# Kernel optimization log

Hardware: AMD Instinct MI355X
Metric: run time of the kernel (lower is better)

The kernel has to match this reference:

```python
import jax, jax.numpy as jnp
import numpy as np
import math

B, A, D = 32, 100, 10000
HID = 256
NH = 4
OUT = 10000
NFREQ = 16
E = round(OUT * 0.5 / (A / 2))  # max_entries = 100
N = int(math.sqrt(D))           # 100 (row/col decode of flat index)
SCALE = math.sqrt(HID)
STEPS = 3


def swish(x):
    return x * jax.nn.sigmoid(x)


def setup_inputs() -> dict:
    key = jax.random.key(0)
    ks = jax.random.split(key, 16)
    s = 0.02
    p = lambda k, shape: jax.random.normal(k, shape, jnp.float32) * s
    vals = jax.random.normal(ks[0], (B, A, D), jnp.float32)
    keep = jax.random.uniform(ks[1], (B, A, D)) < (E / D)  # ~E nonzeros per (b, agent)
    x = vals * keep
    return {
        "x": x,
        "fourier_B": jax.random.normal(ks[2], (NFREQ, 2), jnp.float32),
        "enc_W1": p(ks[3], (HID, 1 + 2 * NFREQ)), "enc_b1": jnp.zeros((HID,), jnp.float32),
        "enc_W2": p(ks[4], (HID, HID)), "enc_b2": jnp.zeros((HID,), jnp.float32),
        "pad_token": jnp.zeros((HID,), jnp.float32),
        "comp_W1": p(ks[5], (2 * HID, E * HID)), "comp_b1": jnp.zeros((2 * HID,), jnp.float32),
        "comp_W2": p(ks[6], (HID, 2 * HID)), "comp_b2": jnp.zeros((HID,), jnp.float32),
        "connectivity": jax.random.normal(ks[7], (A, A), jnp.float32),
        "qW": p(ks[8], (NH, HID, HID)), "kW": p(ks[9], (NH, HID, HID)), "vW": p(ks[10], (NH, HID, HID)),
        "fp_W1": p(ks[11], (NH, HID, HID)), "fp_b1": jnp.zeros((NH, HID), jnp.float32),
        "fp_W2": p(ks[12], (NH, HID, HID)), "fp_b2": jnp.zeros((NH, HID), jnp.float32),
        "ln_g": jnp.ones((NH, HID), jnp.float32), "ln_b": jnp.zeros((NH, HID), jnp.float32),
        "out_W": p(ks[13], (OUT, HID)), "out_b": jnp.zeros((OUT,), jnp.float32),
    }


def reference(x, fourier_B, enc_W1, enc_b1, enc_W2, enc_b2, pad_token,
              comp_W1, comp_b1, comp_W2, comp_b2, connectivity,
              qW, kW, vW, fp_W1, fp_b1, fp_W2, fp_b2, ln_g, ln_b, out_W, out_b):
    # --- ragged gather of nonzero entries, truncated/padded to E per (b, agent) ---
    mask = x != 0                                                   # [B,A,D]
    # stable argsort puts nonzero positions first, in ascending flat-index order
    # (same order as torch .nonzero per batch row)
    idx = jnp.argsort(jnp.logical_not(mask), axis=-1, stable=True)[..., :E]  # [B,A,E]
    valid = jnp.take_along_axis(mask, idx, axis=-1)                 # [B,A,E]
    vals = jnp.take_along_axis(x, idx, axis=-1)[..., None]          # [B,A,E,1]
    coords = jnp.stack([idx // N, idx % N], axis=-1).astype(x.dtype)  # [B,A,E,2]
    # Fourier positional encoding
    proj = (2.0 * math.pi) * jnp.einsum('baec,fc->baef', coords, fourier_B)
    pos = jnp.concatenate([jnp.sin(proj), jnp.cos(proj)], axis=-1)  # [B,A,E,2F]
    feat = jnp.concatenate([vals, pos], axis=-1)                    # [B,A,E,1+2F]
    # entry encoder MLP
    e = swish(feat @ enc_W1.T + enc_b1) @ enc_W2.T + enc_b2         # [B,A,E,HID]
    e = jnp.where(valid[..., None], e, pad_token)                   # pad slots -> pad_token
    # per-agent compression of the E entry embeddings
    flat = e.reshape(B, A, E * HID)
    h = swish(flat @ comp_W1.T + comp_b1) @ comp_W2.T + comp_b2     # [B,A,HID]

    # --- message passing: multi-head dot-product GAT with learned connectivity bias ---
    conn = connectivity[None, None]                                  # broadcast [1,1,A,A]
    for _ in range(STEPS):
        Q = jnp.einsum('bai,nji->nbaj', h, qW)                      # [NH,B,A,HID]
        K = jnp.einsum('bai,nji->nbaj', h, kW)
        V = jnp.einsum('bai,nji->nbaj', h, vW)
        scores = jnp.einsum('nbaj,nbcj->nbac', Q, K) / SCALE + conn
        alpha = jax.nn.softmax(scores, axis=-1)                     # dropout p=0.0
        Hm = jnp.einsum('nbac,nbcj->nbaj', alpha, V)
        t = jnp.einsum('nbaj,nij->nbai', swish(Hm), fp_W1) + fp_b1[:, None, None, :]
        t = jnp.einsum('nbaj,nij->nbai', swish(t), fp_W2) + fp_b2[:, None, None, :]
        m = t.mean(-1, keepdims=True)
        v = ((t - m) ** 2).mean(-1, keepdims=True)
        o = (t - m) / jnp.sqrt(v + 1e-5) * ln_g[:, None, None, :] + ln_b[:, None, None, :]
        h = o.mean(0)                                               # mean over heads

    return h @ out_W.T + out_b                                      # [B,A,OUT]
```

## Files before the change

### kernel.cpp

```cpp
#include <hip/hip_runtime.h>
#include <cstdint>
#include <cstddef>

#define NBATCH 32
#define NAGENT 100
#define NDIM   10000
#define HID    256
#define NHEAD  4
#define NOUT   10000
#define NFREQ  16
#define EMAX   100
#define NBA    3200
#define KBIG   25600
#define TWO_PI 6.283185307179586476925f

typedef float  v4f  __attribute__((ext_vector_type(4)));
typedef short  v8s  __attribute__((ext_vector_type(8)));

__device__ __forceinline__ unsigned short bf_hi(float f) {
    unsigned int u = __float_as_uint(f);
    return (unsigned short)((u + 0x7FFFu + ((u >> 16) & 1u)) >> 16);
}
__device__ __forceinline__ float bf_tof(unsigned short h) {
    return __uint_as_float(((unsigned int)h) << 16);
}

__global__ __launch_bounds__(64) void k_extract(const float* __restrict__ x,
                                                int* __restrict__ idxb,
                                                float* __restrict__ valb,
                                                int* __restrict__ nvalid)
{
    const int ba = blockIdx.x;
    const float* xr = x + (size_t)ba * NDIM;
    const int lane = threadIdx.x;
    int base = 0;
    for (int c0 = 0; c0 < NDIM; c0 += 64) {
        int i = c0 + lane;
        float v = (i < NDIM) ? xr[i] : 0.0f;
        unsigned long long m = __ballot(v != 0.0f);
        if (v != 0.0f) {
            int p = base + __popcll(m & ((1ull << lane) - 1ull));
            if (p < EMAX) {
                idxb[(size_t)ba * EMAX + p] = i;
                valb[(size_t)ba * EMAX + p] = v;
            }
        }
        base += __popcll(m);
        if (base >= EMAX) break;
    }
    if (lane == 0) nvalid[ba] = base < EMAX ? base : EMAX;
}

__global__ __launch_bounds__(256) void k_g1(
    const int* __restrict__ idxb, const float* __restrict__ valb,
    const int* __restrict__ nvalid, const float* __restrict__ fourB,
    const float* __restrict__ W1, const float* __restrict__ b1,
    unsigned short* __restrict__ g1h, unsigned short* __restrict__ g1l)
{
    __shared__ float s_feat[16][36];
    __shared__ float s_w[8448];
    __shared__ float s_b1v[256];
    __shared__ int   s_idx[16];
    __shared__ int   s_valid[16];

    const int t  = threadIdx.x;
    const int g0 = blockIdx.x * 16;

    if (t < 16) {
        int g = g0 + t;
        int ba = g / 100, slot = g - ba * 100;
        int valid = (slot < nvalid[ba]) ? 1 : 0;
        s_valid[t]   = valid;
        s_idx[t]     = valid ? idxb[g] : 0;
        s_feat[t][0] = valid ? valb[g] : 0.0f;
    }
    s_b1v[t] = b1[t];
    for (int i = t; i < 8448; i += 256) s_w[i] = W1[i];
    __syncthreads();

    {
        int ent = t >> 4, f = t & 15;
        float sv = 0.0f, cv = 0.0f;
        if (s_valid[ent]) {
            int id = s_idx[ent];
            float row = (float)(id / 100);
            float col = (float)(id % 100);
            float pr = TWO_PI * (row * fourB[2 * f] + col * fourB[2 * f + 1]);
            sv = sinf(pr); cv = cosf(pr);
        }
        s_feat[ent][1 + f]  = sv;
        s_feat[ent][17 + f] = cv;
    }
    __syncthreads();

    const float* wr = &s_w[t * 33];
    for (int ent = 0; ent < 16; ++ent) {
        float a = s_b1v[t];
        #pragma unroll
        for (int c = 0; c < 33; ++c) a += s_feat[ent][c] * wr[c];
        float g = a / (1.0f + expf(-a));
        g = s_valid[ent] ? g : 0.0f;
        unsigned short h = bf_hi(g);
        unsigned short l = bf_hi(g - bf_tof(h));
        size_t o = (size_t)(g0 + ent) * 256 + t;
        g1h[o] = h;
        g1l[o] = l;
    }
}

__global__ void k_w2t(const float* __restrict__ W2, float* __restrict__ W2T)
{
    int kp = blockIdx.x, k = threadIdx.x;
    W2T[kp * 256 + k] = W2[k * 256 + kp];
}

__global__ __launch_bounds__(256) void k_wsplit(const float* __restrict__ src,
                                                unsigned short* __restrict__ hi,
                                                unsigned short* __restrict__ lo)
{
    int i = (blockIdx.x * 256 + threadIdx.x) * 4;
    float4 f = *(const float4*)(src + i);
    ushort4 h, l;
    h.x = bf_hi(f.x); l.x = bf_hi(f.x - bf_tof(h.x));
    h.y = bf_hi(f.y); l.y = bf_hi(f.y - bf_tof(h.y));
    h.z = bf_hi(f.z); l.z = bf_hi(f.z - bf_tof(h.z));
    h.w = bf_hi(f.w); l.w = bf_hi(f.w - bf_tof(h.w));
    *(ushort4*)(hi + i) = h;
    *(ushort4*)(lo + i) = l;
}

__global__ __launch_bounds__(256) void k_tables(
    const float* __restrict__ W1, const float* __restrict__ pad,
    const float* __restrict__ b2, float* __restrict__ D, float* __restrict__ E0)
{
    __shared__ float red[4];
    const int n = blockIdx.x;
    const int t = threadIdx.x, lane = t & 63, w = t >> 6;
    const float pm = pad[t] - b2[t];
    const float bb = b2[t];
    const float* wr = W1 + (size_t)n * KBIG;
    float eb = 0.0f;
    for (int s = 0; s < 100; ++s) {
        float wv = wr[s * 256 + t];
        float p = pm * wv;
        eb += bb * wv;
        #pragma unroll
        for (int o = 32; o > 0; o >>= 1) p += __shfl_down(p, o);
        if (lane == 0) red[w] = p;
        __syncthreads();
        if (t == 0) D[s * 512 + n] = red[0] + red[1] + red[2] + red[3];
        __syncthreads();
    }
    #pragma unroll
    for (int o = 32; o > 0; o >>= 1) eb += __shfl_down(eb, o);
    if (lane == 0) red[w] = eb;
    __syncthreads();
    if (t == 0) E0[n] = red[0] + red[1] + red[2] + red[3];
}

__global__ void k_suffix(const float* __restrict__ D, float* __restrict__ Corr)
{
    int n = blockIdx.x * 256 + threadIdx.x;
    float c = 0.0f;
    Corr[100 * 512 + n] = 0.0f;
    for (int s = 99; s >= 0; --s) { c += D[s * 512 + n]; Corr[s * 512 + n] = c; }
}

template<int ACT>
__global__ __launch_bounds__(256) void k_gemmbf(
    const unsigned short* __restrict__ Ah, const unsigned short* __restrict__ Al,
    const unsigned short* __restrict__ Wh, const unsigned short* __restrict__ Wl,
    const float* __restrict__ bias, float* __restrict__ C,
    int M, int N, int K,
    long long sA, long long sW, long long sBias, long long sC)
{
    __shared__ unsigned short sA_h[4096], sA_l[4096], sW_h[4096], sW_l[4096];
    const int t = threadIdx.x;
    const int z = blockIdx.z;
    Ah += (size_t)z * sA;  Al += (size_t)z * sA;
    Wh += (size_t)z * sW;  Wl += (size_t)z * sW;
    C  += (size_t)z * sC;
    const float* bp = bias ? (bias + (size_t)z * sBias) : nullptr;
    const int bn = blockIdx.x * 128, bm = blockIdx.y * 128;
    const int lane = t & 63, w = t >> 6;
    const int wm = (w & 1) * 64, wn = (w >> 1) * 64;
    const int r0 = t >> 2, kq = (t & 3) * 8;
    const int r1 = 64 + r0;
    const uint4 zero4 = make_uint4(0u, 0u, 0u, 0u);

    const unsigned short* pA0 = Ah + (size_t)(bm + r0) * K + kq;
    const unsigned short* pA1 = Ah + (size_t)(bm + r1) * K + kq;
    const unsigned short* pa0 = Al + (size_t)(bm + r0) * K + kq;
    const unsigned short* pa1 = Al + (size_t)(bm + r1) * K + kq;
    const bool v0 = (bn + r0) < N, v1 = (bn + r1) < N;
    const unsigned short* pW0 = Wh + (size_t)(bn + r0) * K + kq;
    const unsigned short* pW1 = Wh + (size_t)(bn + r1) * K + kq;
    const unsigned short* pw0 = Wl + (size_t)(bn + r0) * K + kq;
    const unsigned short* pw1 = Wl + (size_t)(bn + r1) * K + kq;

    uint4 rA0 = *(const uint4*)pA0, rA1 = *(const uint4*)pA1;
    uint4 ra0 = *(const uint4*)pa0, ra1 = *(const uint4*)pa1;
    uint4 rW0 = v0 ? *(const uint4*)pW0 : zero4;
    uint4 rW1 = v1 ? *(const uint4*)pW1 : zero4;
    uint4 rw0 = v0 ? *(const uint4*)pw0 : zero4;
    uint4 rw1 = v1 ? *(const uint4*)pw1 : zero4;

    v4f acc[4][4] = {};
    const int i0 = (r0 * 32 + kq) ^ ((r0 & 7) << 3);
    const int i1 = (r1 * 32 + kq) ^ ((r1 & 7) << 3);
    const int KT = K >> 5;

    for (int kt = 0; kt < KT; ++kt) {
        __syncthreads();
        *(uint4*)&sA_h[i0] = rA0;  *(uint4*)&sA_h[i1] = rA1;
        *(uint4*)&sA_l[i0] = ra0;  *(uint4*)&sA_l[i1] = ra1;
        *(uint4*)&sW_h[i0] = rW0;  *(uint4*)&sW_h[i1] = rW1;
        *(uint4*)&sW_l[i0] = rw0;  *(uint4*)&sW_l[i1] = rw1;
        __syncthreads();
        if (kt + 1 < KT) {
            int o = (kt + 1) * 32;
            rA0 = *(const uint4*)(pA0 + o);  rA1 = *(const uint4*)(pA1 + o);
            ra0 = *(const uint4*)(pa0 + o);  ra1 = *(const uint4*)(pa1 + o);
            rW0 = v0 ? *(const uint4*)(pW0 + o) : zero4;
            rW1 = v1 ? *(const uint4*)(pW1 + o) : zero4;
            rw0 = v0 ? *(const uint4*)(pw0 + o) : zero4;
            rw1 = v1 ? *(const uint4*)(pw1 + o) : zero4;
        }
        const int fr = lane & 15, fq = (lane >> 4) * 8;
        v8s ahf[4], alf[4], bhf[4], blf[4];
        #pragma unroll
        for (int i = 0; i < 4; ++i) {
            int ar = wm + i * 16 + fr;
            int br = wn + i * 16 + fr;
            int ai = (ar * 32 + fq) ^ ((ar & 7) << 3);
            int bi = (br * 32 + fq) ^ ((br & 7) << 3);
            ahf[i] = *(const v8s*)&sA_h[ai];
            alf[i] = *(const v8s*)&sA_l[ai];
            bhf[i] = *(const v8s*)&sW_h[bi];
            blf[i] = *(const v8s*)&sW_l[bi];
        }
        #pragma unroll
        for (int mi = 0; mi < 4; ++mi)
            #pragma unroll
            for (int ni = 0; ni < 4; ++ni) {
                acc[mi][ni] = __builtin_amdgcn_mfma_f32_16x16x32_bf16(ahf[mi], bhf[ni], acc[mi][ni], 0, 0, 0);
                acc[mi][ni] = __builtin_amdgcn_mfma_f32_16x16x32_bf16(ahf[mi], blf[ni], acc[mi][ni], 0, 0, 0);
                acc[mi][ni] = __builtin_amdgcn_mfma_f32_16x16x32_bf16(alf[mi], bhf[ni], acc[mi][ni], 0, 0, 0);
            }
    }

    const int er = (lane >> 4) * 4, ec = lane & 15;
    #pragma unroll
    for (int mi = 0; mi < 4; ++mi)
        #pragma unroll
        for (int ni = 0; ni < 4; ++ni) {
            int m = bm + wm + mi * 16 + er;
            int n = bn + wn + ni * 16 + ec;
            if (n < N) {
                float bv = bp ? bp[n] : 0.0f;
                #pragma unroll
                for (int r = 0; r < 4; ++r) {
                    float val = acc[mi][ni][r] + bv;
                    if (ACT == 1) val = val / (1.0f + expf(-val));
                    C[(size_t)(m + r) * N + n] = val;
                }
            }
        }
    (void)M;
}

__global__ __launch_bounds__(256) void k_g3mfma(
    const unsigned short* __restrict__ Ah, const unsigned short* __restrict__ Al,
    const unsigned short* __restrict__ Wh, const unsigned short* __restrict__ Wl,
    float* __restrict__ part)
{
    __shared__ unsigned short sAh[4096], sAl[4096], sWh[4096], sWl[4096];
    const int t  = threadIdx.x;
    const int bn = blockIdx.x * 128;
    const int bm = blockIdx.y * 128;
    const int z  = blockIdx.z;
    const int lane = t & 63, w = t >> 6;
    const int wm = (w & 1) * 64, wn = (w >> 1) * 64;
    const size_t K = KBIG;
    const int r0 = t >> 2, kq = (t & 3) * 8;
    const int r1 = 64 + r0;

    const unsigned short* pA0 = Ah + (size_t)(bm + r0) * K + z * 3200 + kq;
    const unsigned short* pA1 = Ah + (size_t)(bm + r1) * K + z * 3200 + kq;
    const unsigned short* pa0 = Al + (size_t)(bm + r0) * K + z * 3200 + kq;
    const unsigned short* pa1 = Al + (size_t)(bm + r1) * K + z * 3200 + kq;
    const unsigned short* pW0 = Wh + (size_t)(bn + r0) * K + z * 3200 + kq;
    const unsigned short* pW1 = Wh + (size_t)(bn + r1) * K + z * 3200 + kq;
    const unsigned short* pw0 = Wl + (size_t)(bn + r0) * K + z * 3200 + kq;
    const unsigned short* pw1 = Wl + (size_t)(bn + r1) * K + z * 3200 + kq;

    uint4 rA0 = *(const uint4*)pA0, rA1 = *(const uint4*)pA1;
    uint4 ra0 = *(const uint4*)pa0, ra1 = *(const uint4*)pa1;
    uint4 rW0 = *(const uint4*)pW0, rW1 = *(const uint4*)pW1;
    uint4 rw0 = *(const uint4*)pw0, rw1 = *(const uint4*)pw1;

    v4f acc[4][4] = {};
    const int i0 = (r0 * 32 + kq) ^ ((r0 & 7) << 3);
    const int i1 = (r1 * 32 + kq) ^ ((r1 & 7) << 3);

    for (int kt = 0; kt < 100; ++kt) {
        __syncthreads();
        *(uint4*)&sAh[i0] = rA0;  *(uint4*)&sAh[i1] = rA1;
        *(uint4*)&sAl[i0] = ra0;  *(uint4*)&sAl[i1] = ra1;
        *(uint4*)&sWh[i0] = rW0;  *(uint4*)&sWh[i1] = rW1;
        *(uint4*)&sWl[i0] = rw0;  *(uint4*)&sWl[i1] = rw1;
        __syncthreads();
        if (kt < 99) {
            int off = (kt + 1) * 32;
            rA0 = *(const uint4*)(pA0 + off);  rA1 = *(const uint4*)(pA1 + off);
            ra0 = *(const uint4*)(pa0 + off);  ra1 = *(const uint4*)(pa1 + off);
            rW0 = *(const uint4*)(pW0 + off);  rW1 = *(const uint4*)(pW1 + off);
            rw0 = *(const uint4*)(pw0 + off);  rw1 = *(const uint4*)(pw1 + off);
        }
        const int fr = lane & 15, fq = (lane >> 4) * 8;
        v8s ah[4], al[4], bh[4], bl[4];
        #pragma unroll
        for (int i = 0; i < 4; ++i) {
            int ar = wm + i * 16 + fr;
            int br = wn + i * 16 + fr;
            int ai = (ar * 32 + fq) ^ ((ar & 7) << 3);
            int bi = (br * 32 + fq) ^ ((br & 7) << 3);
            ah[i] = *(const v8s*)&sAh[ai];
            al[i] = *(const v8s*)&sAl[ai];
            bh[i] = *(const v8s*)&sWh[bi];
            bl[i] = *(const v8s*)&sWl[bi];
        }
        #pragma unroll
        for (int mi = 0; mi < 4; ++mi)
            #pragma unroll
            for (int ni = 0; ni < 4; ++ni) {
                acc[mi][ni] = __builtin_amdgcn_mfma_f32_16x16x32_bf16(ah[mi], bh[ni], acc[mi][ni], 0, 0, 0);
                acc[mi][ni] = __builtin_amdgcn_mfma_f32_16x16x32_bf16(ah[mi], bl[ni], acc[mi][ni], 0, 0, 0);
                acc[mi][ni] = __builtin_amdgcn_mfma_f32_16x16x32_bf16(al[mi], bh[ni], acc[mi][ni], 0, 0, 0);
            }
    }

    const int er = (lane >> 4) * 4, ec = lane & 15;
    float* cp = part + (size_t)z * NBA * 512;
    #pragma unroll
    for (int mi = 0; mi < 4; ++mi)
        #pragma unroll
        for (int ni = 0; ni < 4; ++ni) {
            int m = bm + wm + mi * 16 + er;
            int n = bn + wn + ni * 16 + ec;
            #pragma unroll
            for (int r = 0; r < 4; ++r)
                cp[(size_t)(m + r) * 512 + n] = acc[mi][ni][r];
        }
}

__global__ __launch_bounds__(256) void k_g3red(
    const float* __restrict__ part, const float* __restrict__ comp_b1,
    const float* __restrict__ E0, const float* __restrict__ Corr,
    const int* __restrict__ nvalid,
    unsigned short* __restrict__ oh, unsigned short* __restrict__ ol)
{
    const int i4 = (blockIdx.x * 256 + threadIdx.x) * 4;
    const int ba = i4 >> 9, n = i4 & 511;
    const size_t S = (size_t)NBA * 512;
    float4 s = *(const float4*)(part + i4);
    #pragma unroll
    for (int zz = 1; zz < 8; ++zz) {
        float4 p = *(const float4*)(part + zz * S + i4);
        s.x += p.x; s.y += p.y; s.z += p.z; s.w += p.w;
    }
    int nv = nvalid[ba];
    float4 b  = *(const float4*)(comp_b1 + n);
    float4 e  = *(const float4*)(E0 + n);
    float4 c  = *(const float4*)(Corr + nv * 512 + n);
    float r0 = s.x + b.x + e.x + c.x;
    float r1 = s.y + b.y + e.y + c.y;
    float r2 = s.z + b.z + e.z + c.z;
    float r3 = s.w + b.w + e.w + c.w;
    float4 o;
    o.x = r0 / (1.0f + expf(-r0));
    o.y = r1 / (1.0f + expf(-r1));
    o.z = r2 / (1.0f + expf(-r2));
    o.w = r3 / (1.0f + expf(-r3));
    ushort4 h, l;
    h.x = bf_hi(o.x); l.x = bf_hi(o.x - bf_tof(h.x));
    h.y = bf_hi(o.y); l.y = bf_hi(o.y - bf_tof(h.y));
    h.z = bf_hi(o.z); l.z = bf_hi(o.z - bf_tof(h.z));
    h.w = bf_hi(o.w); l.w = bf_hi(o.w - bf_tof(h.w));
    *(ushort4*)(oh + i4) = h;
    *(ushort4*)(ol + i4) = l;
}

__global__ __launch_bounds__(256) void k_attn(
    const float* __restrict__ Qb, const float* __restrict__ Kb,
    const float* __restrict__ Vb, const float* __restrict__ conn,
    float* __restrict__ sHm)
{
    __shared__ float sKV[256][101];
    __shared__ float sAl[50][100];
    __shared__ float sQ[2][256];
    __shared__ float sRed[2][2];

    const int t = threadIdx.x;
    const int half = blockIdx.x, b = blockIdx.y, n = blockIdx.z;
    const size_t base = ((size_t)n * NBA + b * 100) * 256;

    const float* Kp = Kb + base;
    for (int r = 0; r < 100; ++r) sKV[t][r] = Kp[(size_t)r * 256 + t];
    __syncthreads();

    const float* Qp = Qb + base;
    const int pair = t >> 7, tt = t & 127, lane = t & 63, wvi = t >> 6;

    for (int rr = 0; rr < 25; ++rr) {
        const int row0 = half * 50 + rr * 2;
        const int lr = rr * 2 + pair;
        __syncthreads();
        sQ[0][t] = Qp[(size_t)(row0)*256 + t];
        sQ[1][t] = Qp[(size_t)(row0 + 1) * 256 + t];
        __syncthreads();
        float sc = 0.0f;
        if (tt < 100) {
            const float* qr = sQ[pair];
            float p0 = 0.f, p1 = 0.f, p2 = 0.f, p3 = 0.f;
            #pragma unroll 4
            for (int c = 0; c < 256; c += 4) {
                p0 += qr[c]     * sKV[c][tt];
                p1 += qr[c + 1] * sKV[c + 1][tt];
                p2 += qr[c + 2] * sKV[c + 2][tt];
                p3 += qr[c + 3] * sKV[c + 3][tt];
            }
            sc = ((p0 + p1) + (p2 + p3)) * 0.0625f + conn[(row0 + pair) * 100 + tt];
            sAl[lr][tt] = sc;
        }
        __syncthreads();
        if ((wvi & 1) == 0) {
            int p = wvi >> 1;
            int r2 = rr * 2 + p;
            float m = sAl[r2][lane];
            if (lane < 36) m = fmaxf(m, sAl[r2][lane + 64]);
            #pragma unroll
            for (int off = 32; off > 0; off >>= 1)
                m = fmaxf(m, __shfl_down(m, off));
            if (lane == 0) sRed[0][p] = m;
        }
        __syncthreads();
        float ex = 0.0f;
        if (tt < 100) {
            ex = expf(sc - sRed[0][pair]);
            sAl[lr][tt] = ex;
        }
        __syncthreads();
        if ((wvi & 1) == 0) {
            int p = wvi >> 1;
            int r2 = rr * 2 + p;
            float s = sAl[r2][lane];
            if (lane < 36) s += sAl[r2][lane + 64];
            #pragma unroll
            for (int off = 32; off > 0; off >>= 1)
                s += __shfl_down(s, off);
            if (lane == 0) sRed[1][p] = s;
        }
        __syncthreads();
        if (tt < 100) sAl[lr][tt] = ex / sRed[1][pair];
    }
    __syncthreads();

    const float* Vp = Vb + base;
    for (int r = 0; r < 100; ++r) sKV[t][r] = Vp[(size_t)r * 256 + t];
    __syncthreads();

    float* Op = sHm + base;
    for (int rr = 0; rr < 50; ++rr) {
        int row = half * 50 + rr;
        float a = 0.0f;
        #pragma unroll 4
        for (int j = 0; j < 100; ++j) a += sAl[rr][j] * sKV[t][j];
        float sw = a / (1.0f + expf(-a));
        Op[(size_t)row * 256 + t] = sw;
    }
}

__global__ __launch_bounds__(256) void k_ln_mean(
    const float* __restrict__ t2b, const float* __restrict__ ln_g,
    const float* __restrict__ ln_b,
    unsigned short* __restrict__ hh, unsigned short* __restrict__ hl)
{
    __shared__ float so[4][256];
    const int ba = blockIdx.x, t = threadIdx.x;
    const int n = t >> 6, lane = t & 63;
    const float* tr = t2b + ((size_t)n * NBA + ba) * HID;
    float4 v = *(const float4*)(tr + lane * 4);
    float s1 = v.x + v.y + v.z + v.w;
    float s2 = v.x * v.x + v.y * v.y + v.z * v.z + v.w * v.w;
    #pragma unroll
    for (int off = 32; off > 0; off >>= 1) {
        s1 += __shfl_down(s1, off);
        s2 += __shfl_down(s2, off);
    }
    s1 = __shfl(s1, 0);
    s2 = __shfl(s2, 0);
    float m = s1 * (1.0f / 256.0f);
    float var = s2 * (1.0f / 256.0f) - m * m;
    float rstd = 1.0f / sqrtf(var + 1e-5f);
    float4 gv = *(const float4*)(ln_g + n * HID + lane * 4);
    float4 bv = *(const float4*)(ln_b + n * HID + lane * 4);
    float4 o;
    o.x = (v.x - m) * rstd * gv.x + bv.x;
    o.y = (v.y - m) * rstd * gv.y + bv.y;
    o.z = (v.z - m) * rstd * gv.z + bv.z;
    o.w = (v.w - m) * rstd * gv.w + bv.w;
    *(float4*)&so[n][lane * 4] = o;
    __syncthreads();
    float hv = 0.25f * (so[0][t] + so[1][t] + so[2][t] + so[3][t]);
    unsigned short hi = bf_hi(hv);
    size_t oidx = (size_t)ba * HID + t;
    hh[oidx] = hi;
    hl[oidx] = bf_hi(hv - bf_tof(hi));
}

extern "C" void kernel_launch(void* const* d_in, const int* in_sizes, int n_in,
                              void* d_out, int out_size, void* d_ws, size_t ws_size,
                              hipStream_t stream)
{
    const float* x       = (const float*)d_in[0];
    const float* fourB   = (const float*)d_in[1];
    const float* enc_W1  = (const float*)d_in[2];
    const float* enc_b1  = (const float*)d_in[3];
    const float* enc_W2  = (const float*)d_in[4];
    const float* enc_b2  = (const float*)d_in[5];
    const float* pad_tok = (const float*)d_in[6];
    const float* comp_W1 = (const float*)d_in[7];
    const float* comp_b1 = (const float*)d_in[8];
    const float* comp_W2 = (const float*)d_in[9];
    const float* comp_b2 = (const float*)d_in[10];
    const float* conn    = (const float*)d_in[11];
    const float* qW      = (const float*)d_in[12];
    const float* kW      = (const float*)d_in[13];
    const float* vW      = (const float*)d_in[14];
    const float* fpW1    = (const float*)d_in[15];
    const float* fpb1    = (const float*)d_in[16];
    const float* fpW2    = (const float*)d_in[17];
    const float* fpb2    = (const float*)d_in[18];
    const float* ln_g    = (const float*)d_in[19];
    const float* ln_b    = (const float*)d_in[20];
    const float* out_W   = (const float*)d_in[21];
    const float* out_b   = (const float*)d_in[22];
    float* outp = (float*)d_out;

    char* ws = (char*)d_ws;
    size_t off = 0;
    auto alloc = [&](size_t bytes) -> void* {
        void* p = (void*)(ws + off);
        off += (bytes + 255) & ~(size_t)255;
        return p;
    };
    int*   idxb = (int*)  alloc((size_t)NBA * EMAX * 4);
    float* valb = (float*)alloc((size_t)NBA * EMAX * 4);
    int*   nval = (int*)  alloc((size_t)NBA * 4);
    unsigned short* g1h = (unsigned short*)alloc((size_t)NBA * KBIG * 2);
    unsigned short* g1l = (unsigned short*)alloc((size_t)NBA * KBIG * 2);
    float* W2T  = (float*)alloc((size_t)256 * 256 * 4);
    float* W1p  = (float*)alloc((size_t)512 * KBIG * 4);
    float* part = W1p;
    unsigned short* Whi = (unsigned short*)alloc((size_t)512 * KBIG * 2);
    unsigned short* Wlo = (unsigned short*)alloc((size_t)512 * KBIG * 2);
    float* Dt   = (float*)alloc((size_t)100 * 512 * 4);
    float* Corr = (float*)alloc((size_t)101 * 512 * 4);
    float* E0   = (float*)alloc((size_t)512 * 4);
    float* h    = (float*)alloc((size_t)NBA * HID * 4);
    float* Qb   = (float*)alloc((size_t)NHEAD * NBA * HID * 4);
    float* Kb   = (float*)alloc((size_t)NHEAD * NBA * HID * 4);
    float* Vb   = (float*)alloc((size_t)NHEAD * NBA * HID * 4);
    unsigned short* asplh = (unsigned short*)alloc((size_t)NHEAD * NBA * HID * 2);
    unsigned short* aspll = (unsigned short*)alloc((size_t)NHEAD * NBA * HID * 2);
    unsigned short* cW1h = (unsigned short*)Qb;
    unsigned short* cW1l = (unsigned short*)Vb;
    unsigned short* w2tH = (unsigned short*)alloc((size_t)256 * 256 * 2);
    unsigned short* w2tL = (unsigned short*)alloc((size_t)256 * 256 * 2);
    unsigned short* qkvWh = (unsigned short*)alloc((size_t)3 * NHEAD * HID * HID * 2);
    unsigned short* qkvWl = (unsigned short*)alloc((size_t)3 * NHEAD * HID * HID * 2);
    unsigned short* f1Wh = (unsigned short*)alloc((size_t)NHEAD * HID * HID * 2);
    unsigned short* f1Wl = (unsigned short*)alloc((size_t)NHEAD * HID * HID * 2);
    unsigned short* f2Wh = (unsigned short*)alloc((size_t)NHEAD * HID * HID * 2);
    unsigned short* f2Wl = (unsigned short*)alloc((size_t)NHEAD * HID * HID * 2);
    unsigned short* c2Wh = (unsigned short*)alloc((size_t)HID * 512 * 2);
    unsigned short* c2Wl = (unsigned short*)alloc((size_t)HID * 512 * 2);
    unsigned short* oWh  = (unsigned short*)alloc((size_t)NOUT * HID * 2);
    unsigned short* oWl  = (unsigned short*)alloc((size_t)NOUT * HID * 2);
    float* sHmB = Qb;
    float* t1s  = Kb;
    float* t2b  = Vb;

    const long long sW = (long long)HID * HID;
    const long long sC = (long long)NBA * HID;

    k_extract<<<NBA, 64, 0, stream>>>(x, idxb, valb, nval);
    k_g1<<<NBA * EMAX / 16, 256, 0, stream>>>(idxb, valb, nval, fourB,
                                              enc_W1, enc_b1, g1h, g1l);

    k_w2t<<<256, 256, 0, stream>>>(enc_W2, W2T);
    k_wsplit<<<256 * 256 / 1024, 256, 0, stream>>>(W2T, w2tH, w2tL);
    k_wsplit<<<512 * KBIG / 1024, 256, 0, stream>>>(comp_W1, cW1h, cW1l);
    k_gemmbf<0><<<dim3(2, 400, 1), 256, 0, stream>>>(
        cW1h, cW1l, w2tH, w2tL, nullptr, W1p, 512 * EMAX, 256, 256, 0, 0, 0, 0);
    k_wsplit<<<512 * KBIG / 1024, 256, 0, stream>>>(W1p, Whi, Wlo);
    k_tables<<<512, 256, 0, stream>>>(comp_W1, pad_tok, enc_b2, Dt, E0);
    k_suffix<<<2, 256, 0, stream>>>(Dt, Corr);

    k_wsplit<<<NHEAD * 65536 / 1024, 256, 0, stream>>>(qW, qkvWh, qkvWl);
    k_wsplit<<<NHEAD * 65536 / 1024, 256, 0, stream>>>(kW, qkvWh + NHEAD * 65536, qkvWl + NHEAD * 65536);
    k_wsplit<<<NHEAD * 65536 / 1024, 256, 0, stream>>>(vW, qkvWh + 2 * NHEAD * 65536, qkvWl + 2 * NHEAD * 65536);
    k_wsplit<<<NHEAD * 65536 / 1024, 256, 0, stream>>>(fpW1, f1Wh, f1Wl);
    k_wsplit<<<NHEAD * 65536 / 1024, 256, 0, stream>>>(fpW2, f2Wh, f2Wl);
    k_wsplit<<<HID * 512 / 1024, 256, 0, stream>>>(comp_W2, c2Wh, c2Wl);
    k_wsplit<<<NOUT * HID / 1024, 256, 0, stream>>>(out_W, oWh, oWl);

    k_g3mfma<<<dim3(4, 25, 8), 256, 0, stream>>>(g1h, g1l, Whi, Wlo, part);
    k_g3red<<<NBA * 512 / 1024, 256, 0, stream>>>(part, comp_b1, E0, Corr, nval, asplh, aspll);
    k_gemmbf<0><<<dim3(2, 25, 1), 256, 0, stream>>>(
        asplh, aspll, c2Wh, c2Wl, comp_b2, h, NBA, HID, 512, 0, 0, 0, 0);
    k_wsplit<<<NBA * HID / 1024, 256, 0, stream>>>(h, asplh, aspll);

    for (int step = 0; step < 3; ++step) {
        k_gemmbf<0><<<dim3(2, 25, 12), 256, 0, stream>>>(
            asplh, aspll, qkvWh, qkvWl, nullptr, Qb, NBA, HID, HID, 0, sW, 0, sC);
        k_attn<<<dim3(2, NBATCH, NHEAD), 256, 0, stream>>>(Qb, Kb, Vb, conn, sHmB);
        k_wsplit<<<NHEAD * NBA * HID / 1024, 256, 0, stream>>>(sHmB, asplh, aspll);
        k_gemmbf<1><<<dim3(2, 25, 4), 256, 0, stream>>>(
            asplh, aspll, f1Wh, f1Wl, fpb1, t1s, NBA, HID, HID, sC, sW, HID, sC);
        k_wsplit<<<NHEAD * NBA * HID / 1024, 256, 0, stream>>>(t1s, asplh, aspll);
        k_gemmbf<0><<<dim3(2, 25, 4), 256, 0, stream>>>(
            asplh, aspll, f2Wh, f2Wl, fpb2, t2b, NBA, HID, HID, sC, sW, HID, sC);
        k_ln_mean<<<NBA, 256, 0, stream>>>(t2b, ln_g, ln_b, asplh, aspll);
    }

    k_gemmbf<0><<<dim3(79, 25, 1), 256, 0, stream>>>(
        asplh, aspll, oWh, oWl, out_b, outp, NBA, NOUT, HID, 0, 0, 0, 0);

    (void)in_sizes; (void)n_in; (void)out_size; (void)ws_size;
}
```

Baseline: 1.985 ms.

## Fuse bf16 hi/lo splitting into GEMM and attention epilogues; remap g3 block order

Measured after the change: 1.905 ms. -4.1%, faster.

```diff
diff --git a/kernel.cpp b/kernel.cpp
--- a/kernel.cpp
+++ b/kernel.cpp
@@ -166,11 +166,12 @@
     for (int s = 99; s >= 0; --s) { c += D[s * 512 + n]; Corr[s * 512 + n] = c; }
 }
 
-template<int ACT>
+template<int ACT, int SPLIT>
 __global__ __launch_bounds__(256) void k_gemmbf(
     const unsigned short* __restrict__ Ah, const unsigned short* __restrict__ Al,
     const unsigned short* __restrict__ Wh, const unsigned short* __restrict__ Wl,
     const float* __restrict__ bias, float* __restrict__ C,
+    unsigned short* __restrict__ Ch, unsigned short* __restrict__ Cl,
     int M, int N, int K,
     long long sA, long long sW, long long sBias, long long sC)
 {
@@ -179,7 +180,8 @@
     const int z = blockIdx.z;
     Ah += (size_t)z * sA;  Al += (size_t)z * sA;
     Wh += (size_t)z * sW;  Wl += (size_t)z * sW;
-    C  += (size_t)z * sC;
+    if (SPLIT) { Ch += (size_t)z * sC; Cl += (size_t)z * sC; }
+    else       { C  += (size_t)z * sC; }
     const float* bp = bias ? (bias + (size_t)z * sBias) : nullptr;
     const int bn = blockIdx.x * 128, bm = blockIdx.y * 128;
     const int lane = t & 63, w = t >> 6;
@@ -262,7 +264,13 @@
                 for (int r = 0; r < 4; ++r) {
                     float val = acc[mi][ni][r] + bv;
                     if (ACT == 1) val = val / (1.0f + expf(-val));
-                    C[(size_t)(m + r) * N + n] = val;
+                    if (SPLIT) {
+                        unsigned short hv = bf_hi(val);
+                        Ch[(size_t)(m + r) * N + n] = hv;
+                        Cl[(size_t)(m + r) * N + n] = bf_hi(val - bf_tof(hv));
+                    } else {
+                        C[(size_t)(m + r) * N + n] = val;
+                    }
                 }
             }
         }
@@ -276,9 +284,11 @@
 {
     __shared__ unsigned short sAh[4096], sAl[4096], sWh[4096], sWl[4096];
     const int t  = threadIdx.x;
-    const int bn = blockIdx.x * 128;
-    const int bm = blockIdx.y * 128;
-    const int z  = blockIdx.z;
+    const int hwid = blockIdx.x;
+    const int wk = (hwid & 7) * 100 + (hwid >> 3);
+    const int bn = (wk & 3) * 128;
+    const int bm = ((wk >> 2) % 25) * 128;
+    const int z  = wk / 100;
     const int lane = t & 63, w = t >> 6;
     const int wm = (w & 1) * 64, wn = (w >> 1) * 64;
     const size_t K = KBIG;
@@ -394,7 +404,7 @@
 __global__ __launch_bounds__(256) void k_attn(
     const float* __restrict__ Qb, const float* __restrict__ Kb,
     const float* __restrict__ Vb, const float* __restrict__ conn,
-    float* __restrict__ sHm)
+    unsigned short* __restrict__ Oh, unsigned short* __restrict__ Ol)
 {
     __shared__ float sKV[256][101];
     __shared__ float sAl[50][100];
@@ -470,14 +480,16 @@
     for (int r = 0; r < 100; ++r) sKV[t][r] = Vp[(size_t)r * 256 + t];
     __syncthreads();
 
-    float* Op = sHm + base;
     for (int rr = 0; rr < 50; ++rr) {
         int row = half * 50 + rr;
         float a = 0.0f;
         #pragma unroll 4
         for (int j = 0; j < 100; ++j) a += sAl[rr][j] * sKV[t][j];
         float sw = a / (1.0f + expf(-a));
-        Op[(size_t)row * 256 + t] = sw;
+        size_t oidx = base + (size_t)row * 256 + t;
+        unsigned short hv = bf_hi(sw);
+        Oh[oidx] = hv;
+        Ol[oidx] = bf_hi(sw - bf_tof(hv));
     }
 }
 
@@ -568,7 +580,6 @@
     float* Dt   = (float*)alloc((size_t)100 * 512 * 4);
     float* Corr = (float*)alloc((size_t)101 * 512 * 4);
     float* E0   = (float*)alloc((size_t)512 * 4);
-    float* h    = (float*)alloc((size_t)NBA * HID * 4);
     float* Qb   = (float*)alloc((size_t)NHEAD * NBA * HID * 4);
     float* Kb   = (float*)alloc((size_t)NHEAD * NBA * HID * 4);
     float* Vb   = (float*)alloc((size_t)NHEAD * NBA * HID * 4);
@@ -576,6 +587,8 @@
     unsigned short* aspll = (unsigned short*)alloc((size_t)NHEAD * NBA * HID * 2);
     unsigned short* cW1h = (unsigned short*)Qb;
     unsigned short* cW1l = (unsigned short*)Vb;
+    unsigned short* bsplh = g1h;
+    unsigned short* bspll = g1h + (size_t)NHEAD * NBA * HID;
     unsigned short* w2tH = (unsigned short*)alloc((size_t)256 * 256 * 2);
     unsigned short* w2tL = (unsigned short*)alloc((size_t)256 * 256 * 2);
     unsigned short* qkvWh = (unsigned short*)alloc((size_t)3 * NHEAD * HID * HID * 2);
@@ -588,8 +601,6 @@
     unsigned short* c2Wl = (unsigned short*)alloc((size_t)HID * 512 * 2);
     unsigned short* oWh  = (unsigned short*)alloc((size_t)NOUT * HID * 2);
     unsigned short* oWl  = (unsigned short*)alloc((size_t)NOUT * HID * 2);
-    float* sHmB = Qb;
-    float* t1s  = Kb;
     float* t2b  = Vb;
 
     const long long sW = (long long)HID * HID;
@@ -602,8 +613,9 @@
     k_w2t<<<256, 256, 0, stream>>>(enc_W2, W2T);
     k_wsplit<<<256 * 256 / 1024, 256, 0, stream>>>(W2T, w2tH, w2tL);
     k_wsplit<<<512 * KBIG / 1024, 256, 0, stream>>>(comp_W1, cW1h, cW1l);
-    k_gemmbf<0><<<dim3(2, 400, 1), 256, 0, stream>>>(
-        cW1h, cW1l, w2tH, w2tL, nullptr, W1p, 512 * EMAX, 256, 256, 0, 0, 0, 0);
+    k_gemmbf<0, 0><<<dim3(2, 400, 1), 256, 0, stream>>>(
+        cW1h, cW1l, w2tH, w2tL, nullptr, W1p, nullptr, nullptr,
+        512 * EMAX, 256, 256, 0, 0, 0, 0);
     k_wsplit<<<512 * KBIG / 1024, 256, 0, stream>>>(W1p, Whi, Wlo);
     k_tables<<<512, 256, 0, stream>>>(comp_W1, pad_tok, enc_b2, Dt, E0);
     k_suffix<<<2, 256, 0, stream>>>(Dt, Corr);
@@ -616,27 +628,29 @@
     k_wsplit<<<HID * 512 / 1024, 256, 0, stream>>>(comp_W2, c2Wh, c2Wl);
     k_wsplit<<<NOUT * HID / 1024, 256, 0, stream>>>(out_W, oWh, oWl);
 
-    k_g3mfma<<<dim3(4, 25, 8), 256, 0, stream>>>(g1h, g1l, Whi, Wlo, part);
+    k_g3mfma<<<800, 256, 0, stream>>>(g1h, g1l, Whi, Wlo, part);
     k_g3red<<<NBA * 512 / 1024, 256, 0, stream>>>(part, comp_b1, E0, Corr, nval, asplh, aspll);
-    k_gemmbf<0><<<dim3(2, 25, 1), 256, 0, stream>>>(
-        asplh, aspll, c2Wh, c2Wl, comp_b2, h, NBA, HID, 512, 0, 0, 0, 0);
-    k_wsplit<<<NBA * HID / 1024, 256, 0, stream>>>(h, asplh, aspll);
+    k_gemmbf<0, 1><<<dim3(2, 25, 1), 256, 0, stream>>>(
+        asplh, aspll, c2Wh, c2Wl, comp_b2, nullptr, bsplh, bspll,
+        NBA, HID, 512, 0, 0, 0, 0);
 
     for (int step = 0; step < 3; ++step) {
-        k_gemmbf<0><<<dim3(2, 25, 12), 256, 0, stream>>>(
-            asplh, aspll, qkvWh, qkvWl, nullptr, Qb, NBA, HID, HID, 0, sW, 0, sC);
-        k_attn<<<dim3(2, NBATCH, NHEAD), 256, 0, stream>>>(Qb, Kb, Vb, conn, sHmB);
-        k_wsplit<<<NHEAD * NBA * HID / 1024, 256, 0, stream>>>(sHmB, asplh, aspll);
-        k_gemmbf<1><<<dim3(2, 25, 4), 256, 0, stream>>>(
-            asplh, aspll, f1Wh, f1Wl, fpb1, t1s, NBA, HID, HID, sC, sW, HID, sC);
-        k_wsplit<<<NHEAD * NBA * HID / 1024, 256, 0, stream>>>(t1s, asplh, aspll);
-        k_gemmbf<0><<<dim3(2, 25, 4), 256, 0, stream>>>(
-            asplh, aspll, f2Wh, f2Wl, fpb2, t2b, NBA, HID, HID, sC, sW, HID, sC);
-        k_ln_mean<<<NBA, 256, 0, stream>>>(t2b, ln_g, ln_b, asplh, aspll);
-    }
-
-    k_gemmbf<0><<<dim3(79, 25, 1), 256, 0, stream>>>(
-        asplh, aspll, oWh, oWl, out_b, outp, NBA, NOUT, HID, 0, 0, 0, 0);
+        k_gemmbf<0, 0><<<dim3(2, 25, 12), 256, 0, stream>>>(
+            bsplh, bspll, qkvWh, qkvWl, nullptr, Qb, nullptr, nullptr,
+            NBA, HID, HID, 0, sW, 0, sC);
+        k_attn<<<dim3(2, NBATCH, NHEAD), 256, 0, stream>>>(Qb, Kb, Vb, conn, asplh, aspll);
+        k_gemmbf<1, 1><<<dim3(2, 25, 4), 256, 0, stream>>>(
+            asplh, aspll, f1Wh, f1Wl, fpb1, nullptr, bsplh, bspll,
+            NBA, HID, HID, sC, sW, HID, sC);
+        k_gemmbf<0, 0><<<dim3(2, 25, 4), 256, 0, stream>>>(
+            bsplh, bspll, f2Wh, f2Wl, fpb2, t2b, nullptr, nullptr,
+            NBA, HID, HID, sC, sW, HID, sC);
+        k_ln_mean<<<NBA, 256, 0, stream>>>(t2b, ln_g, ln_b, bsplh, bspll);
+    }
+
+    k_gemmbf<0, 0><<<dim3(79, 25, 1), 256, 0, stream>>>(
+        bsplh, bspll, oWh, oWl, out_b, outp, nullptr, nullptr,
+        NBA, NOUT, HID, 0, 0, 0, 0);
 
     (void)in_sizes; (void)n_in; (void)out_size; (void)ws_size;
 }
```
